# Performance work log

Hardware: AMD Instinct MI355X
Metric: run time of the kernel (lower is better)

## Reference

```python
import jax, jax.numpy as jnp
import numpy as np

EPS = 1e-8  # torch nn.CosineSimilarity default eps


def setup_inputs() -> dict:
    key = jax.random.key(0)
    k1, k2 = jax.random.split(key)
    support_set = jax.random.normal(k1, (50000, 512), dtype=jnp.float32)
    query_set = jax.random.normal(k2, (2048, 512), dtype=jnp.float32)
    return {"support_set": support_set, "query_set": query_set}


def reference(support_set, query_set):
    # torch: cos(x1, x2) = x1.x2 / max(||x1|| * ||x2||, eps), per row.
    # Loop over queries fused into one matmul: out[q, n] = cos(support[n], query[q]).
    dots = jnp.einsum("qd,nd->qn", query_set, support_set)        # [Q, N]
    s_norm = jnp.linalg.norm(support_set, axis=1)                  # [N]
    q_norm = jnp.linalg.norm(query_set, axis=1)                    # [Q]
    denom = jnp.maximum(q_norm[:, None] * s_norm[None, :], EPS)    # [Q, N]
    return dots / denom
```

## Files before the change

kernel.cpp:

```cpp
#include <hip/hip_runtime.h>
#include <stdint.h>

#define NSUP   50000
#define NSUPP  50176
#define NQRY   2048
#define KD     512
#define BK     32
#define NKT    16

typedef __attribute__((ext_vector_type(8))) short bf16x8;
typedef __attribute__((ext_vector_type(4))) float f32x4;

__device__ __forceinline__ unsigned short f2bf(float f) {
  unsigned int u = __float_as_uint(f);
  u += 0x7FFFu + ((u >> 16) & 1u);
  return (unsigned short)(u >> 16);
}

__global__ __launch_bounds__(256) void prep_kernel(
    const float* __restrict__ sup, const float* __restrict__ qry,
    unsigned short* __restrict__ s_bf, unsigned short* __restrict__ q_bf) {
  const int row  = blockIdx.x * 4 + (threadIdx.x >> 6);
  const int lane = threadIdx.x & 63;

  const float* src = nullptr;
  unsigned short* dst;
  if (row < NSUPP) {
    dst = s_bf + (size_t)row * KD;
    if (row < NSUP) src = sup + (size_t)row * KD;
  } else {
    const int r = row - NSUPP;
    dst = q_bf + (size_t)r * KD;
    src = qry + (size_t)r * KD;
  }

  if (src == nullptr) {
    bf16x8 z = {};
    *(bf16x8*)(dst + lane * 8) = z;
    return;
  }

  const float4 v0 = ((const float4*)src)[lane * 2 + 0];
  const float4 v1 = ((const float4*)src)[lane * 2 + 1];
  float ss = v0.x*v0.x + v0.y*v0.y + v0.z*v0.z + v0.w*v0.w
           + v1.x*v1.x + v1.y*v1.y + v1.z*v1.z + v1.w*v1.w;
  #pragma unroll
  for (int off = 32; off > 0; off >>= 1) ss += __shfl_xor(ss, off);
  const float inv = rsqrtf(fmaxf(ss, 1e-30f));

  bf16x8 o;
  o[0]=(short)f2bf(v0.x*inv); o[1]=(short)f2bf(v0.y*inv);
  o[2]=(short)f2bf(v0.z*inv); o[3]=(short)f2bf(v0.w*inv);
  o[4]=(short)f2bf(v1.x*inv); o[5]=(short)f2bf(v1.y*inv);
  o[6]=(short)f2bf(v1.z*inv); o[7]=(short)f2bf(v1.w*inv);
  *(bf16x8*)(dst + lane * 8) = o;
}

__device__ __forceinline__ void stage_unit(const unsigned short* __restrict__ g,
                                           unsigned short* lds, int grow_base,
                                           int kt, int w, int l) {
  const int chunk = (l & 3) ^ ((l >> 3) & 3);
  #pragma unroll
  for (int i = 0; i < 2; ++i) {
    const unsigned short* src = g + (size_t)(grow_base + i*64 + w*16 + (l>>2)) * KD
                                  + kt*BK + chunk*8;
    unsigned short* dst = lds + i*2048 + w*512;
    __builtin_amdgcn_global_load_lds(
        (const __attribute__((address_space(1))) void*)src,
        (__attribute__((address_space(3))) void*)dst, 16, 0, 0);
  }
}

#define SWZ_OFF(R, hi) (((hi) ^ (((R) >> 1) & 3)) * 8)

__global__ __launch_bounds__(256, 3) void gemm_kernel(
    const unsigned short* __restrict__ S,
    const unsigned short* __restrict__ Q,
    float* __restrict__ out) {
  __shared__ __attribute__((aligned(16))) unsigned short As[2][128][BK];
  __shared__ __attribute__((aligned(16))) unsigned short Bs[2][128][BK];

  const int tid = threadIdx.x;
  const int w = tid >> 6, l = tid & 63;
  const int wr = w >> 1, wc = w & 1;
  const int rof = l & 15, hi = l >> 4;

  int bid = blockIdx.y * 392 + blockIdx.x;
  bid = (bid & 7) * 784 + (bid >> 3);
  const int ts = (bid % 392) * 128;
  const int tq = (bid / 392) * 128;

  f32x4 acc[4][4] = {};

  stage_unit(S, &As[0][0][0], ts, 0, w, l);
  stage_unit(Q, &Bs[0][0][0], tq, 0, w, l);
  __syncthreads();

  #pragma unroll
  for (int t = 0; t < NKT; ++t) {
    const int slot = t & 1;
    if (t + 1 < NKT) {
      stage_unit(S, &As[slot ^ 1][0][0], ts, t + 1, w, l);
      stage_unit(Q, &Bs[slot ^ 1][0][0], tq, t + 1, w, l);
    }

    bf16x8 a[4], b[4];
    #pragma unroll
    for (int i = 0; i < 4; ++i) {
      const int R = wr*64 + i*16 + rof;
      a[i] = *(const bf16x8*)&As[slot][R][SWZ_OFF(R, hi)];
    }
    #pragma unroll
    for (int i = 0; i < 4; ++i) {
      const int R = wc*64 + i*16 + rof;
      b[i] = *(const bf16x8*)&Bs[slot][R][SWZ_OFF(R, hi)];
    }

    #pragma unroll
    for (int mi = 0; mi < 4; ++mi)
      #pragma unroll
      for (int ni = 0; ni < 4; ++ni)
        acc[mi][ni] = __builtin_amdgcn_mfma_f32_16x16x32_bf16(a[mi], b[ni], acc[mi][ni], 0, 0, 0);

    __syncthreads();
  }

  #pragma unroll
  for (int mi = 0; mi < 4; ++mi) {
    const int s = ts + wr*64 + mi*16 + hi*4;
    if (s < NSUP) {
      #pragma unroll
      for (int ni = 0; ni < 4; ++ni) {
        const int q = tq + wc*64 + ni*16 + rof;
        *(f32x4*)(out + (size_t)q * NSUP + s) = acc[mi][ni];
      }
    }
  }
}

extern "C" void kernel_launch(void* const* d_in, const int* in_sizes, int n_in,
                              void* d_out, int out_size, void* d_ws, size_t ws_size,
                              hipStream_t stream) {
  const float* sup = (const float*)d_in[0];
  const float* qry = (const float*)d_in[1];
  float* out = (float*)d_out;

  char* ws = (char*)d_ws;
  unsigned short* s_bf = (unsigned short*)(ws);
  unsigned short* q_bf = (unsigned short*)(ws + (size_t)NSUPP * KD * 2);

  prep_kernel<<<(NSUPP + NQRY) / 4, 256, 0, stream>>>(sup, qry, s_bf, q_bf);

  dim3 grid(392, 16);
  gemm_kernel<<<grid, 256, 0, stream>>>(s_bf, q_bf, out);
}
```

Before: 246.5 us.

## Enlarge GEMM tile to 256x512 per 512-thread block with nontemporal output stores

Replaces the 128x128 block tile (256 threads, 4x4 MFMA tiles per wave) with a 256-support by 512-query tile run by 8 waves, each owning a 128x128 sub-tile of 8x8 MFMA accumulators. This raises data reuse per LDS load and cuts global re-reads of the bf16 inputs. It moves LDS to dynamic shared memory, drops the block-index swizzle and the k-loop unroll, and writes output with nontemporal stores to avoid cache pollution on the large fp32 result. The trade-off is very high register pressure (256 accumulator registers per lane), only one block per CU with less latency hiding, and a coarser grid with tail imbalance.

```diff
diff --git a/kernel.cpp b/kernel.cpp
--- a/kernel.cpp
+++ b/kernel.cpp
@@ -7,6 +7,8 @@
 #define KD     512
 #define BK     32
 #define NKT    16
+#define BQ     512
+#define BS     256
 
 typedef __attribute__((ext_vector_type(8))) short bf16x8;
 typedef __attribute__((ext_vector_type(4))) float f32x4;
@@ -56,83 +58,84 @@
   *(bf16x8*)(dst + lane * 8) = o;
 }
 
+template<int RPW>
 __device__ __forceinline__ void stage_unit(const unsigned short* __restrict__ g,
                                            unsigned short* lds, int grow_base,
                                            int kt, int w, int l) {
   const int chunk = (l & 3) ^ ((l >> 3) & 3);
   #pragma unroll
-  for (int i = 0; i < 2; ++i) {
-    const unsigned short* src = g + (size_t)(grow_base + i*64 + w*16 + (l>>2)) * KD
-                                  + kt*BK + chunk*8;
-    unsigned short* dst = lds + i*2048 + w*512;
+  for (int i = 0; i < RPW / 16; ++i) {
+    const int rb = w * RPW + i * 16;
+    const unsigned short* src = g + (size_t)(grow_base + rb + (l >> 2)) * KD
+                                  + kt * BK + chunk * 8;
+    unsigned short* dst = lds + rb * BK + l * 8;
     __builtin_amdgcn_global_load_lds(
         (const __attribute__((address_space(1))) void*)src,
         (__attribute__((address_space(3))) void*)dst, 16, 0, 0);
   }
 }
 
-#define SWZ_OFF(R, hi) (((hi) ^ (((R) >> 1) & 3)) * 8)
-
-__global__ __launch_bounds__(256, 3) void gemm_kernel(
+__global__ __launch_bounds__(512, 1) void gemm_kernel(
     const unsigned short* __restrict__ S,
     const unsigned short* __restrict__ Q,
     float* __restrict__ out) {
-  __shared__ __attribute__((aligned(16))) unsigned short As[2][128][BK];
-  __shared__ __attribute__((aligned(16))) unsigned short Bs[2][128][BK];
+  extern __shared__ unsigned short sm[];
+  unsigned short* Qs = sm;
+  unsigned short* Ss = sm + 2 * BQ * BK;
 
   const int tid = threadIdx.x;
   const int w = tid >> 6, l = tid & 63;
-  const int wr = w >> 1, wc = w & 1;
+  const int ws = w & 1, wq = w >> 1;
   const int rof = l & 15, hi = l >> 4;
+  const int gsw = hi ^ ((rof >> 1) & 3);
 
-  int bid = blockIdx.y * 392 + blockIdx.x;
-  bid = (bid & 7) * 784 + (bid >> 3);
-  const int ts = (bid % 392) * 128;
-  const int tq = (bid / 392) * 128;
+  const int ts = blockIdx.x * BS;
+  const int tq = blockIdx.y * BQ;
 
-  f32x4 acc[4][4] = {};
+  f32x4 acc[8][8] = {};
 
-  stage_unit(S, &As[0][0][0], ts, 0, w, l);
-  stage_unit(Q, &Bs[0][0][0], tq, 0, w, l);
+  stage_unit<BQ/8>(Q, Qs, tq, 0, w, l);
+  stage_unit<BS/8>(S, Ss, ts, 0, w, l);
   __syncthreads();
 
-  #pragma unroll
+  #pragma unroll 1
   for (int t = 0; t < NKT; ++t) {
-    const int slot = t & 1;
+    const int cur = t & 1;
     if (t + 1 < NKT) {
-      stage_unit(S, &As[slot ^ 1][0][0], ts, t + 1, w, l);
-      stage_unit(Q, &Bs[slot ^ 1][0][0], tq, t + 1, w, l);
+      stage_unit<BQ/8>(Q, Qs + (cur ^ 1) * BQ * BK, tq, t + 1, w, l);
+      stage_unit<BS/8>(S, Ss + (cur ^ 1) * BS * BK, ts, t + 1, w, l);
     }
 
-    bf16x8 a[4], b[4];
+    bf16x8 a[8], b[8];
     #pragma unroll
-    for (int i = 0; i < 4; ++i) {
-      const int R = wr*64 + i*16 + rof;
-      a[i] = *(const bf16x8*)&As[slot][R][SWZ_OFF(R, hi)];
+    for (int si = 0; si < 8; ++si) {
+      const int R = ws * 128 + si * 16 + rof;
+      a[si] = *(const bf16x8*)(Ss + cur * BS * BK + R * BK + gsw * 8);
     }
     #pragma unroll
-    for (int i = 0; i < 4; ++i) {
-      const int R = wc*64 + i*16 + rof;
-      b[i] = *(const bf16x8*)&Bs[slot][R][SWZ_OFF(R, hi)];
+    for (int qi = 0; qi < 8; ++qi) {
+      const int R = wq * 128 + qi * 16 + rof;
+      b[qi] = *(const bf16x8*)(Qs + cur * BQ * BK + R * BK + gsw * 8);
     }
 
     #pragma unroll
-    for (int mi = 0; mi < 4; ++mi)
+    for (int si = 0; si < 8; ++si)
       #pragma unroll
-      for (int ni = 0; ni < 4; ++ni)
-        acc[mi][ni] = __builtin_amdgcn_mfma_f32_16x16x32_bf16(a[mi], b[ni], acc[mi][ni], 0, 0, 0);
+      for (int qi = 0; qi < 8; ++qi)
+        acc[si][qi] = __builtin_amdgcn_mfma_f32_16x16x32_bf16(a[si], b[qi], acc[si][qi], 0, 0, 0);
 
     __syncthreads();
   }
 
   #pragma unroll
-  for (int mi = 0; mi < 4; ++mi) {
-    const int s = ts + wr*64 + mi*16 + hi*4;
+  for (int si = 0; si < 8; ++si) {
+    const int s = ts + ws * 128 + si * 16 + hi * 4;
     if (s < NSUP) {
       #pragma unroll
-      for (int ni = 0; ni < 4; ++ni) {
-        const int q = tq + wc*64 + ni*16 + rof;
-        *(f32x4*)(out + (size_t)q * NSUP + s) = acc[mi][ni];
+      for (int qi = 0; qi < 8; ++qi) {
+        const int q = tq + wq * 128 + qi * 16 + rof;
+        __builtin_nontemporal_store(acc[si][qi],
+                                    (f32x4*)(out + (size_t)q * NSUP + s));
       }
     }
   }
@@ -151,6 +154,7 @@
 
   prep_kernel<<<(NSUPP + NQRY) / 4, 256, 0, stream>>>(sup, qry, s_bf, q_bf);
 
-  dim3 grid(392, 16);
-  gemm_kernel<<<grid, 256, 0, stream>>>(s_bf, q_bf, out);
+  dim3 grid(NSUPP / BS, NQRY / BQ);
+  const size_t lds_bytes = (2 * BQ * BK + 2 * BS * BK) * sizeof(unsigned short);
+  gemm_kernel<<<grid, 512, lds_bytes, stream>>>(s_bf, q_bf, out);
 }
```

Measured after the change: 737.1 us. 199% more time.
